# Optimization experiments

Hardware: AMD Instinct MI355X
Metric: run time of the kernel (lower is better)

Reference implementation:

```python
import jax, jax.numpy as jnp
import numpy as np

B, S, D, NH = 1024, 128, 512, 8
DH = D // NH  # head dim = 64


def setup_inputs() -> dict:
    key = jax.random.key(0)
    ks = jax.random.split(key, 9)
    scale = 1.0 / np.sqrt(D)
    return {
        "x_non": jax.random.normal(ks[0], (B, D), jnp.float32),
        "x_seq": jax.random.normal(ks[1], (B, S, D), jnp.float32),
        "mask": jax.random.randint(ks[2], (B, NH, S), 0, 2, jnp.int32),
        "Wq": jax.random.normal(ks[3], (D, D), jnp.float32) * scale,
        "bq": jax.random.normal(ks[4], (D,), jnp.float32) * scale,
        "Wk": jax.random.normal(ks[5], (D, D), jnp.float32) * scale,
        "bk": jax.random.normal(ks[6], (D,), jnp.float32) * scale,
        "Wv": jax.random.normal(ks[7], (D, D), jnp.float32) * scale,
        "bv": jax.random.normal(ks[8], (D,), jnp.float32) * scale,
    }


def reference(x_non, x_seq, mask, Wq, bq, Wk, bk, Wv, bv):
    batch, seq_len, dim = x_seq.shape
    nhead = NH
    dh = dim // nhead
    # Linear projections (torch Linear: y = x @ W.T + b)
    q = (x_non @ Wq.T + bq).reshape(batch, nhead, dh)           # (b, n, d)
    k = (x_seq @ Wk.T + bk).reshape(batch, seq_len, nhead, dh)  # (b, s, n, d)
    v = (x_seq @ Wv.T + bv).reshape(batch, seq_len, nhead, dh)
    qk = jnp.einsum("bnd,bsnd->bns", q, k)
    # NOTE: source uses `//` (floor division) by sqrt(d_head) -- reproduced faithfully
    qk = jnp.floor(qk / jnp.sqrt(jnp.asarray(dh, qk.dtype)))
    qk = jnp.where(mask == 0, jnp.asarray(-1e9, qk.dtype), qk)
    attn = jax.nn.softmax(qk, axis=-1)                           # (b, n, s)
    z = jnp.einsum("bns,bsnd->bnd", attn, v).reshape(batch, dim)
    return z
```

## Files before the change

kernel.cpp:

```cpp
#include <hip/hip_runtime.h>

#define SS  128
#define DD  512
#define NHH 8
#define DHH 64

typedef float  f4 __attribute__((ext_vector_type(4)));
typedef float  f2 __attribute__((ext_vector_type(2)));
typedef double d2 __attribute__((ext_vector_type(2)));

typedef const void __attribute__((address_space(1)))* gas_t;
typedef void __attribute__((address_space(3)))* las_t;

__global__ __launch_bounds__(256) void qproj_kernel(
    const float* __restrict__ x_non, const float* __restrict__ Wq,
    const float* __restrict__ bq, double* __restrict__ qws)
{
    const int tid = threadIdx.x;
    const int bt  = blockIdx.x & 31;
    const int ot  = blockIdx.x >> 5;
    const int r   = tid >> 4, c = tid & 15;

    __shared__ __attribute__((aligned(16))) float Xs[32][68];
    __shared__ __attribute__((aligned(16))) float Ws[64][68];

    double acc[2][4];
    #pragma unroll
    for (int i = 0; i < 2; ++i)
        #pragma unroll
        for (int j = 0; j < 4; ++j) acc[i][j] = 0.0;

    for (int kc = 0; kc < 8; ++kc) {
        __syncthreads();
        #pragma unroll
        for (int p = 0; p < 2; ++p) {
            int s = tid + 256 * p, rr = s >> 4, cc = (s & 15) * 4;
            *(f4*)&Xs[rr][cc] = *(const f4*)(x_non + (size_t)(bt * 32 + rr) * DD + kc * 64 + cc);
        }
        #pragma unroll
        for (int p = 0; p < 4; ++p) {
            int s = tid + 256 * p, rr = s >> 4, cc = (s & 15) * 4;
            *(f4*)&Ws[rr][cc] = *(const f4*)(Wq + (size_t)(ot * 64 + rr) * DD + kc * 64 + cc);
        }
        __syncthreads();
        #pragma unroll 4
        for (int kk = 0; kk < 64; ++kk) {
            double a0 = (double)Xs[r][kk];
            double a1 = (double)Xs[r + 16][kk];
            #pragma unroll
            for (int j = 0; j < 4; ++j) {
                double bb = (double)Ws[c + 16 * j][kk];
                acc[0][j] = fma(a0, bb, acc[0][j]);
                acc[1][j] = fma(a1, bb, acc[1][j]);
            }
        }
    }
    #pragma unroll
    for (int i = 0; i < 2; ++i)
        #pragma unroll
        for (int j = 0; j < 4; ++j) {
            int o = ot * 64 + c + 16 * j;
            qws[(size_t)(bt * 32 + r + 16 * i) * DD + o] = acc[i][j] + (double)bq[o];
        }
}

__device__ __forceinline__ void stage_chunk(const float* __restrict__ Xb,
                                            int c, int buf, int tid, float* XsF)
{
    const int wid  = tid >> 6;
    const int lane = tid & 63;
    const float* gsrc = Xb + (size_t)c * (8 * DD);
    #pragma unroll
    for (int p = 0; p < 4; ++p) {
        const int gbase = p * 256 + wid * 64;
        const float* gp = gsrc + (size_t)(gbase + lane) * 4;
        float* lp = XsF + (size_t)buf * 4096 + (size_t)gbase * 4;
        __builtin_amdgcn_global_load_lds((gas_t)gp, (las_t)lp, 16, 0, 0);
    }
}

__global__ __launch_bounds__(256) void core_kernel(
    const double* __restrict__ qws, const float* __restrict__ x_seq,
    const int* __restrict__ mask, const float* __restrict__ Wk,
    const float* __restrict__ bk, float* __restrict__ uws)
{
    const int tid = threadIdx.x;
    const int b   = blockIdx.x;
    const float* Xb = x_seq + (size_t)b * (SS * DD);

    const int hp    = tid >> 6;
    const int rhalf = (tid >> 5) & 1;
    const int k16   = tid & 31;

    __shared__ __attribute__((aligned(16))) union {
        double T[8][512];
        float  Xs[2][8][512];
    } sh;
    __shared__ __attribute__((aligned(16))) union {
        double qd[512];
        int    mk[1024];
    } sh2;
    __shared__ double qbks[8];

    float* XsF = &sh.Xs[0][0][0];

    sh2.qd[tid]       = qws[(size_t)b * DD + tid];
    sh2.qd[tid + 256] = qws[(size_t)b * DD + tid + 256];
    __syncthreads();

    if (tid < 64) {
        const int h = tid >> 3, part = tid & 7;
        double s = 0.0;
        #pragma unroll
        for (int ii = 0; ii < 8; ++ii) {
            int d = part * 8 + ii;
            s = fma(sh2.qd[h * DHH + d], (double)bk[h * DHH + d], s);
        }
        s += __shfl_xor(s, 1);
        s += __shfl_xor(s, 2);
        s += __shfl_xor(s, 4);
        if (part == 0) qbks[h] = s;
    }

    {
        const int kg = tid & 127, dh = tid >> 7;
        const int k4 = kg * 4;
        for (int hg = 0; hg < 2; ++hg) {
            double tacc[4][4];
            #pragma unroll
            for (int h4 = 0; h4 < 4; ++h4) {
                const int h = hg * 4 + h4;
                const float* wp = Wk + ((size_t)(h * DHH + dh * 32)) * DD + k4;
                double t0 = 0, t1 = 0, t2 = 0, t3 = 0;
                for (int d = 0; d < 32; ++d) {
                    f4 wv = *(const f4*)(wp + (size_t)d * DD);
                    double qv = sh2.qd[h * DHH + dh * 32 + d];
                    t0 = fma((double)wv[0], qv, t0);
                    t1 = fma((double)wv[1], qv, t1);
                    t2 = fma((double)wv[2], qv, t2);
                    t3 = fma((double)wv[3], qv, t3);
                }
                tacc[h4][0] = t0; tacc[h4][1] = t1; tacc[h4][2] = t2; tacc[h4][3] = t3;
            }
            if (dh == 1) {
                #pragma unroll
                for (int h4 = 0; h4 < 4; ++h4)
                    #pragma unroll
                    for (int e = 0; e < 4; ++e)
                        sh.T[hg * 4 + h4][k4 + e] = tacc[h4][e];
            }
            __syncthreads();
            if (dh == 0) {
                #pragma unroll
                for (int h4 = 0; h4 < 4; ++h4)
                    #pragma unroll
                    for (int e = 0; e < 4; ++e)
                        sh.T[hg * 4 + h4][k4 + e] += tacc[h4][e];
            }
            __syncthreads();
        }
    }

    d2 treg[2][8];
    #pragma unroll
    for (int hh = 0; hh < 2; ++hh)
        #pragma unroll
        for (int p = 0; p < 8; ++p)
            treg[hh][p] = *(const d2*)&sh.T[hp * 2 + hh][k16 * 2 + 64 * p];
    float qbkf[2] = { (float)qbks[hp * 2], (float)qbks[hp * 2 + 1] };
    __syncthreads();

    #pragma unroll
    for (int p = 0; p < 4; ++p)
        sh2.mk[tid + 256 * p] = mask[(size_t)b * (NHH * SS) + tid + 256 * p];
    stage_chunk(Xb, 0, 0, tid, XsF);
    asm volatile("s_waitcnt vmcnt(0)");
    __syncthreads();

    float u[2][16];
    #pragma unroll
    for (int hh = 0; hh < 2; ++hh)
        #pragma unroll
        for (int j = 0; j < 16; ++j) u[hh][j] = 0.f;
    float m_run[2] = { -1e30f, -1e30f };
    float l_run[2] = { 0.f, 0.f };

    for (int c = 0; c < 16; ++c) {
        const int buf = c & 1;
        if (c < 15) stage_chunk(Xb, c + 1, buf ^ 1, tid, XsF);

        const float* Xc = XsF + buf * 4096 + (rhalf * 4) * DD + k16 * 2;

        double acc[2][4];
        #pragma unroll
        for (int hh = 0; hh < 2; ++hh)
            #pragma unroll
            for (int r = 0; r < 4; ++r) acc[hh][r] = 0.0;

        #pragma unroll
        for (int r = 0; r < 4; ++r) {
            #pragma unroll
            for (int p = 0; p < 8; ++p) {
                f2 xv = *(const f2*)&Xc[r * DD + p * 64];
                double x0 = (double)xv[0], x1 = (double)xv[1];
                #pragma unroll
                for (int hh = 0; hh < 2; ++hh) {
                    acc[hh][r] = fma(x0, treg[hh][p][0], acc[hh][r]);
                    acc[hh][r] = fma(x1, treg[hh][p][1], acc[hh][r]);
                }
            }
        }

        float Lown[2][4];
        #pragma unroll
        for (int hh = 0; hh < 2; ++hh)
            #pragma unroll
            for (int r = 0; r < 4; ++r) {
                float s = (float)acc[hh][r];
                s += __shfl_xor(s, 1);
                s += __shfl_xor(s, 2);
                s += __shfl_xor(s, 4);
                s += __shfl_xor(s, 8);
                s += __shfl_xor(s, 16);
                s = floorf((s + qbkf[hh]) * 0.125f);
                const int row = c * 8 + rhalf * 4 + r;
                if (sh2.mk[(hp * 2 + hh) * SS + row] == 0) s = -1e9f;
                Lown[hh][r] = s;
            }

        float pw[2][4];
        #pragma unroll
        for (int hh = 0; hh < 2; ++hh) {
            float Loth[4];
            #pragma unroll
            for (int r = 0; r < 4; ++r) Loth[r] = __shfl_xor(Lown[hh][r], 32);
            float cmax = fmaxf(
                fmaxf(fmaxf(Lown[hh][0], Lown[hh][1]), fmaxf(Lown[hh][2], Lown[hh][3])),
                fmaxf(fmaxf(Loth[0], Loth[1]), fmaxf(Loth[2], Loth[3])));
            float mnew = fmaxf(m_run[hh], cmax);
            if (mnew != m_run[hh]) {
                float fs = __expf(m_run[hh] - mnew);
                #pragma unroll
                for (int j = 0; j < 16; ++j) u[hh][j] *= fs;
                l_run[hh] *= fs;
                m_run[hh] = mnew;
            }
            float ps = 0.f;
            #pragma unroll
            for (int r = 0; r < 4; ++r) { pw[hh][r] = __expf(Lown[hh][r] - mnew); ps += pw[hh][r]; }
            #pragma unroll
            for (int r = 0; r < 4; ++r) ps += __expf(Loth[r] - mnew);
            l_run[hh] += ps;
        }

        #pragma unroll
        for (int r = 0; r < 4; ++r) {
            #pragma unroll
            for (int p = 0; p < 8; ++p) {
                f2 xv = *(const f2*)&Xc[r * DD + p * 64];
                #pragma unroll
                for (int hh = 0; hh < 2; ++hh) {
                    u[hh][p * 2]     = fmaf(pw[hh][r], xv[0], u[hh][p * 2]);
                    u[hh][p * 2 + 1] = fmaf(pw[hh][r], xv[1], u[hh][p * 2 + 1]);
                }
            }
        }

        asm volatile("s_waitcnt vmcnt(0)");
        __syncthreads();
    }

    #pragma unroll
    for (int hh = 0; hh < 2; ++hh)
        #pragma unroll
        for (int j = 0; j < 16; ++j) u[hh][j] += __shfl_xor(u[hh][j], 32);

    {
        const int h = hp * 2 + rhalf;
        const float inv = 1.0f / (rhalf ? l_run[1] : l_run[0]);
        float* dst = uws + ((size_t)b * NHH + h) * DD + k16 * 2;
        #pragma unroll
        for (int p = 0; p < 8; ++p) {
            f2 v;
            v[0] = (rhalf ? u[1][p * 2]     : u[0][p * 2])     * inv;
            v[1] = (rhalf ? u[1][p * 2 + 1] : u[0][p * 2 + 1]) * inv;
            *(f2*)&dst[p * 64] = v;
        }
    }
}

__global__ __launch_bounds__(256) void zout_kernel(
    const float* __restrict__ uws, const float* __restrict__ Wv,
    const float* __restrict__ bv, float* __restrict__ out)
{
    const int tid = threadIdx.x;
    const int bt  = blockIdx.x & 31;
    const int ot  = blockIdx.x >> 5;
    const int r   = tid >> 4, c = tid & 15;

    __shared__ __attribute__((aligned(16))) float Us[32][68];
    __shared__ __attribute__((aligned(16))) float Ws[64][68];

    float acc[2][4];
    #pragma unroll
    for (int i = 0; i < 2; ++i)
        #pragma unroll
        for (int j = 0; j < 4; ++j) acc[i][j] = 0.f;

    for (int kc = 0; kc < 8; ++kc) {
        __syncthreads();
        #pragma unroll
        for (int p = 0; p < 2; ++p) {
            int s = tid + 256 * p, rr = s >> 4, cc = (s & 15) * 4;
            *(f4*)&Us[rr][cc] =
                *(const f4*)(uws + ((size_t)(bt * 32 + rr) * NHH + ot) * DD + kc * 64 + cc);
        }
        #pragma unroll
        for (int p = 0; p < 4; ++p) {
            int s = tid + 256 * p, rr = s >> 4, cc = (s & 15) * 4;
            *(f4*)&Ws[rr][cc] = *(const f4*)(Wv + (size_t)(ot * 64 + rr) * DD + kc * 64 + cc);
        }
        __syncthreads();
        #pragma unroll 4
        for (int kk = 0; kk < 64; ++kk) {
            float a0 = Us[r][kk];
            float a1 = Us[r + 16][kk];
            #pragma unroll
            for (int j = 0; j < 4; ++j) {
                float bb = Ws[c + 16 * j][kk];
                acc[0][j] = fmaf(a0, bb, acc[0][j]);
                acc[1][j] = fmaf(a1, bb, acc[1][j]);
            }
        }
    }
    #pragma unroll
    for (int i = 0; i < 2; ++i)
        #pragma unroll
        for (int j = 0; j < 4; ++j) {
            int o = ot * 64 + c + 16 * j;
            out[(size_t)(bt * 32 + r + 16 * i) * DD + o] = acc[i][j] + bv[o];
        }
}

extern "C" void kernel_launch(void* const* d_in, const int* in_sizes, int n_in,
                              void* d_out, int out_size, void* d_ws, size_t ws_size,
                              hipStream_t stream) {
    const float* x_non = (const float*)d_in[0];
    const float* x_seq = (const float*)d_in[1];
    const int*   mask  = (const int*)d_in[2];
    const float* Wq    = (const float*)d_in[3];
    const float* bq    = (const float*)d_in[4];
    const float* Wk    = (const float*)d_in[5];
    const float* bk    = (const float*)d_in[6];
    const float* Wv    = (const float*)d_in[7];
    const float* bv    = (const float*)d_in[8];
    float*       out   = (float*)d_out;

    double* qws = (double*)d_ws;
    float*  uws = (float*)((char*)d_ws + (size_t)1024 * DD * 8);

    qproj_kernel<<<256, 256, 0, stream>>>(x_non, Wq, bq, qws);
    core_kernel<<<1024, 256, 0, stream>>>(qws, x_seq, mask, Wk, bk, uws);
    zout_kernel<<<256, 256, 0, stream>>>(uws, Wv, bv, out);
}
```

Baseline: 490.1 us.

## Fuse Q projection and output projection into single per-batch attention kernel

Merges the three launches into one kernel. Each block computes its query row as a wave-level fp64 GEMV over Wq, runs the existing attention core, and then computes its output row as a wave-level GEMV over Wv from shared memory. This removes the workspace round trips and two launches. In exchange, every block streams the full Wq and Wv matrices and does 64-lane shuffle reductions per output, which greatly raises per-block work and L2 traffic.

```diff
diff --git a/kernel.cpp b/kernel.cpp
--- a/kernel.cpp
+++ b/kernel.cpp
@@ -11,58 +11,6 @@
 
 typedef const void __attribute__((address_space(1)))* gas_t;
 typedef void __attribute__((address_space(3)))* las_t;
-
-__global__ __launch_bounds__(256) void qproj_kernel(
-    const float* __restrict__ x_non, const float* __restrict__ Wq,
-    const float* __restrict__ bq, double* __restrict__ qws)
-{
-    const int tid = threadIdx.x;
-    const int bt  = blockIdx.x & 31;
-    const int ot  = blockIdx.x >> 5;
-    const int r   = tid >> 4, c = tid & 15;
-
-    __shared__ __attribute__((aligned(16))) float Xs[32][68];
-    __shared__ __attribute__((aligned(16))) float Ws[64][68];
-
-    double acc[2][4];
-    #pragma unroll
-    for (int i = 0; i < 2; ++i)
-        #pragma unroll
-        for (int j = 0; j < 4; ++j) acc[i][j] = 0.0;
-
-    for (int kc = 0; kc < 8; ++kc) {
-        __syncthreads();
-        #pragma unroll
-        for (int p = 0; p < 2; ++p) {
-            int s = tid + 256 * p, rr = s >> 4, cc = (s & 15) * 4;
-            *(f4*)&Xs[rr][cc] = *(const f4*)(x_non + (size_t)(bt * 32 + rr) * DD + kc * 64 + cc);
-        }
-        #pragma unroll
-        for (int p = 0; p < 4; ++p) {
-            int s = tid + 256 * p, rr = s >> 4, cc = (s & 15) * 4;
-            *(f4*)&Ws[rr][cc] = *(const f4*)(Wq + (size_t)(ot * 64 + rr) * DD + kc * 64 + cc);
-        }
-        __syncthreads();
-        #pragma unroll 4
-        for (int kk = 0; kk < 64; ++kk) {
-            double a0 = (double)Xs[r][kk];
-            double a1 = (double)Xs[r + 16][kk];
-            #pragma unroll
-            for (int j = 0; j < 4; ++j) {
-                double bb = (double)Ws[c + 16 * j][kk];
-                acc[0][j] = fma(a0, bb, acc[0][j]);
-                acc[1][j] = fma(a1, bb, acc[1][j]);
-            }
-        }
-    }
-    #pragma unroll
-    for (int i = 0; i < 2; ++i)
-        #pragma unroll
-        for (int j = 0; j < 4; ++j) {
-            int o = ot * 64 + c + 16 * j;
-            qws[(size_t)(bt * 32 + r + 16 * i) * DD + o] = acc[i][j] + (double)bq[o];
-        }
-}
 
 __device__ __forceinline__ void stage_chunk(const float* __restrict__ Xb,
                                             int c, int buf, int tid, float* XsF)
@@ -79,10 +27,13 @@
     }
 }
 
-__global__ __launch_bounds__(256) void core_kernel(
-    const double* __restrict__ qws, const float* __restrict__ x_seq,
-    const int* __restrict__ mask, const float* __restrict__ Wk,
-    const float* __restrict__ bk, float* __restrict__ uws)
+__global__ __launch_bounds__(256, 4) void fused_kernel(
+    const float* __restrict__ x_non, const float* __restrict__ x_seq,
+    const int* __restrict__ mask,
+    const float* __restrict__ Wq, const float* __restrict__ bq,
+    const float* __restrict__ Wk, const float* __restrict__ bk,
+    const float* __restrict__ Wv, const float* __restrict__ bv,
+    float* __restrict__ out)
 {
     const int tid = threadIdx.x;
     const int b   = blockIdx.x;
@@ -91,21 +42,57 @@
     const int hp    = tid >> 6;
     const int rhalf = (tid >> 5) & 1;
     const int k16   = tid & 31;
+    const int wid   = tid >> 6;
+    const int lane  = tid & 63;
 
     __shared__ __attribute__((aligned(16))) union {
         double T[8][512];
         float  Xs[2][8][512];
+        float  U[8][512];
     } sh;
     __shared__ __attribute__((aligned(16))) union {
         double qd[512];
         int    mk[1024];
     } sh2;
     __shared__ double qbks[8];
+    __shared__ __attribute__((aligned(16))) float xns[512];
 
     float* XsF = &sh.Xs[0][0][0];
 
-    sh2.qd[tid]       = qws[(size_t)b * DD + tid];
-    sh2.qd[tid + 256] = qws[(size_t)b * DD + tid + 256];
+    xns[tid]       = x_non[(size_t)b * DD + tid];
+    xns[tid + 256] = x_non[(size_t)b * DD + tid + 256];
+    __syncthreads();
+
+    {
+        double xd[8];
+        {
+            f4 xa = *(const f4*)&xns[lane * 8];
+            f4 xb = *(const f4*)&xns[lane * 8 + 4];
+            xd[0] = (double)xa[0]; xd[1] = (double)xa[1];
+            xd[2] = (double)xa[2]; xd[3] = (double)xa[3];
+            xd[4] = (double)xb[0]; xd[5] = (double)xb[1];
+            xd[6] = (double)xb[2]; xd[7] = (double)xb[3];
+        }
+        #pragma unroll 2
+        for (int i = 0; i < 128; ++i) {
+            const int o = wid * 128 + i;
+            const float* wp = Wq + (size_t)o * DD + lane * 8;
+            f4 wa = *(const f4*)wp;
+            f4 wb = *(const f4*)(wp + 4);
+            double a = 0.0;
+            a = fma((double)wa[0], xd[0], a);
+            a = fma((double)wa[1], xd[1], a);
+            a = fma((double)wa[2], xd[2], a);
+            a = fma((double)wa[3], xd[3], a);
+            a = fma((double)wb[0], xd[4], a);
+            a = fma((double)wb[1], xd[5], a);
+            a = fma((double)wb[2], xd[6], a);
+            a = fma((double)wb[3], xd[7], a);
+            #pragma unroll
+            for (int off = 1; off < 64; off <<= 1) a += __shfl_xor(a, off);
+            if (lane == 0) sh2.qd[o] = a + (double)bq[o];
+        }
+    }
     __syncthreads();
 
     if (tid < 64) {
@@ -278,68 +265,41 @@
     {
         const int h = hp * 2 + rhalf;
         const float inv = 1.0f / (rhalf ? l_run[1] : l_run[0]);
-        float* dst = uws + ((size_t)b * NHH + h) * DD + k16 * 2;
         #pragma unroll
         for (int p = 0; p < 8; ++p) {
             f2 v;
             v[0] = (rhalf ? u[1][p * 2]     : u[0][p * 2])     * inv;
             v[1] = (rhalf ? u[1][p * 2 + 1] : u[0][p * 2 + 1]) * inv;
-            *(f2*)&dst[p * 64] = v;
-        }
-    }
-}
-
-__global__ __launch_bounds__(256) void zout_kernel(
-    const float* __restrict__ uws, const float* __restrict__ Wv,
-    const float* __restrict__ bv, float* __restrict__ out)
-{
-    const int tid = threadIdx.x;
-    const int bt  = blockIdx.x & 31;
-    const int ot  = blockIdx.x >> 5;
-    const int r   = tid >> 4, c = tid & 15;
-
-    __shared__ __attribute__((aligned(16))) float Us[32][68];
-    __shared__ __attribute__((aligned(16))) float Ws[64][68];
-
-    float acc[2][4];
-    #pragma unroll
-    for (int i = 0; i < 2; ++i)
-        #pragma unroll
-        for (int j = 0; j < 4; ++j) acc[i][j] = 0.f;
-
-    for (int kc = 0; kc < 8; ++kc) {
-        __syncthreads();
-        #pragma unroll
-        for (int p = 0; p < 2; ++p) {
-            int s = tid + 256 * p, rr = s >> 4, cc = (s & 15) * 4;
-            *(f4*)&Us[rr][cc] =
-                *(const f4*)(uws + ((size_t)(bt * 32 + rr) * NHH + ot) * DD + kc * 64 + cc);
-        }
-        #pragma unroll
-        for (int p = 0; p < 4; ++p) {
-            int s = tid + 256 * p, rr = s >> 4, cc = (s & 15) * 4;
-            *(f4*)&Ws[rr][cc] = *(const f4*)(Wv + (size_t)(ot * 64 + rr) * DD + kc * 64 + cc);
-        }
-        __syncthreads();
-        #pragma unroll 4
-        for (int kk = 0; kk < 64; ++kk) {
-            float a0 = Us[r][kk];
-            float a1 = Us[r + 16][kk];
-            #pragma unroll
-            for (int j = 0; j < 4; ++j) {
-                float bb = Ws[c + 16 * j][kk];
-                acc[0][j] = fmaf(a0, bb, acc[0][j]);
-                acc[1][j] = fmaf(a1, bb, acc[1][j]);
-            }
-        }
-    }
-    #pragma unroll
-    for (int i = 0; i < 2; ++i)
-        #pragma unroll
-        for (int j = 0; j < 4; ++j) {
-            int o = ot * 64 + c + 16 * j;
-            out[(size_t)(bt * 32 + r + 16 * i) * DD + o] = acc[i][j] + bv[o];
-        }
+            *(f2*)&sh.U[h][k16 * 2 + p * 64] = v;
+        }
+    }
+    __syncthreads();
+
+    #pragma unroll
+    for (int hh2 = 0; hh2 < 2; ++hh2) {
+        const int h = wid * 2 + hh2;
+        f4 ua = *(const f4*)&sh.U[h][lane * 8];
+        f4 ub = *(const f4*)&sh.U[h][lane * 8 + 4];
+        #pragma unroll 2
+        for (int j = 0; j < 64; ++j) {
+            const int o = h * 64 + j;
+            const float* wp = Wv + (size_t)o * DD + lane * 8;
+            f4 wa = *(const f4*)wp;
+            f4 wb = *(const f4*)(wp + 4);
+            float a = 0.f;
+            a = fmaf(wa[0], ua[0], a);
+            a = fmaf(wa[1], ua[1], a);
+            a = fmaf(wa[2], ua[2], a);
+            a = fmaf(wa[3], ua[3], a);
+            a = fmaf(wb[0], ub[0], a);
+            a = fmaf(wb[1], ub[1], a);
+            a = fmaf(wb[2], ub[2], a);
+            a = fmaf(wb[3], ub[3], a);
+            #pragma unroll
+            for (int off = 1; off < 64; off <<= 1) a += __shfl_xor(a, off);
+            if (lane == 0) out[(size_t)b * DD + o] = a + bv[o];
+        }
+    }
 }
 
 extern "C" void kernel_launch(void* const* d_in, const int* in_sizes, int n_in,
@@ -356,10 +316,6 @@
     const float* bv    = (const float*)d_in[8];
     float*       out   = (float*)d_out;
 
-    double* qws = (double*)d_ws;
-    float*  uws = (float*)((char*)d_ws + (size_t)1024 * DD * 8);
-
-    qproj_kernel<<<256, 256, 0, stream>>>(x_non, Wq, bq, qws);
-    core_kernel<<<1024, 256, 0, stream>>>(qws, x_seq, mask, Wk, bk, uws);
-    zout_kernel<<<256, 256, 0, stream>>>(uws, Wv, bv, out);
+    fused_kernel<<<1024, 256, 0, stream>>>(x_non, x_seq, mask,
+                                           Wq, bq, Wk, bk, Wv, bv, out);
 }
```

New measurement: 748.7 us. 1.53x slower.
